# Performance work log

Measured on AMD Instinct MI355X. Metric: run time of the kernel, lower is better.

## Reference

```python
import jax, jax.numpy as jnp
import numpy as np

EPS = 1e-8


def setup_inputs() -> dict:
    key = jax.random.key(0)
    k1, k2, k3, k4 = jax.random.split(key, 4)
    B, D, K, L = 131072, 256, 1024, 526
    points = jax.random.normal(k1, (B, D), dtype=jnp.float32)
    labels = jax.random.uniform(k2, (B, L), dtype=jnp.float32)
    centroids = jax.random.normal(k3, (K, D), dtype=jnp.float32)
    running_labels = jax.random.uniform(k4, (K, L), dtype=jnp.float32)
    return {"points": points, "labels": labels, "centroids": centroids,
            "running_labels": running_labels}


def reference(points, labels, centroids, running_labels):
    # One kmeans step: assign -> compute_distance -> compute_distance_labels -> update
    K = centroids.shape[0]
    B = points.shape[0]
    # compute_similarity: squared euclidean distance (B, K), fused matmul form
    x2 = jnp.sum(points * points, axis=-1, keepdims=True)          # (B, 1)
    c2 = jnp.sum(centroids * centroids, axis=-1)                   # (K,)
    d = x2 - 2.0 * (points @ centroids.T) + c2                     # (B, K)
    assignment = jnp.argmin(d, axis=1)                             # (B,)

    # compute_distance: squared dist to assigned centroid + per-cluster dispersion
    sel = centroids[assignment]                                    # (B, D) gather
    dist = jnp.sum(jnp.square(sel - points), axis=-1)              # (B,)
    dispersion = jax.ops.segment_sum(dist, assignment, num_segments=K)

    # compute_distance_labels: cosine distance to assigned cluster label profile
    cl = running_labels[assignment]                                # (B, L) gather
    norm = jnp.sqrt(jnp.sum(jnp.square(labels), axis=-1))
    norm1 = jnp.sqrt(jnp.sum(jnp.square(cl), axis=-1))
    dist_labels = 1.0 - jnp.sum(cl * labels, axis=-1) / (norm * norm1 + EPS)
    dispersion_labels = jax.ops.segment_sum(dist_labels, assignment, num_segments=K)

    # update: scatter segment-sum running statistics
    new_sum = jax.ops.segment_sum(points, assignment, num_segments=K)   # (K, D)
    new_n = jax.ops.segment_sum(jnp.ones((B,), points.dtype), assignment, num_segments=K)
    new_labels = jax.ops.segment_sum(labels, assignment, num_segments=K)  # (K, L)

    return (assignment, dist, dispersion, dist_labels, dispersion_labels,
            new_sum, new_n, new_labels)
```

## Files before the change

kernel.cpp:

```cpp
#include <hip/hip_runtime.h>
#include <float.h>
#include <math.h>

constexpr int Bn = 131072;
constexpr int Dn = 256;
constexpr int Kn = 1024;
constexpr int Ln = 526;
constexpr float EPSF = 1e-8f;

constexpr int CHUNK = 128;
constexpr int MAXCHUNKS = Bn / CHUNK + Kn;

constexpr int BM  = 128;
constexpr int BN  = 128;
constexpr int KC  = 32;
constexpr int NT  = Kn / BN;
constexpr int KCH = Dn / KC;
constexpr int NCH = NT * KCH;
constexpr int LDH = 40;

typedef _Float16 f16x8 __attribute__((ext_vector_type(8)));
typedef _Float16 f16x4 __attribute__((ext_vector_type(4)));
typedef float    f32x4 __attribute__((ext_vector_type(4)));

union SMemU {
    _Float16 planes[2][4][BM][LDH];
    struct { float t[BM][2]; int k[BM][2]; } red;
};

__global__ __launch_bounds__(256) void prep_kernel(
    const float* __restrict__ centroids, const float* __restrict__ rlabels,
    float* __restrict__ c2, float* __restrict__ rln)
{
    const int k = blockIdx.x;
    const int t = threadIdx.x;
    float v = centroids[k * Dn + t];
    float s1 = v * v;
    float s2 = 0.f;
    for (int i = t; i < Ln; i += 256) {
        float u = rlabels[(size_t)k * Ln + i];
        s2 += u * u;
    }
    for (int off = 32; off > 0; off >>= 1) {
        s1 += __shfl_down(s1, off, 64);
        s2 += __shfl_down(s2, off, 64);
    }
    __shared__ float red[8];
    const int wv = t >> 6;
    if ((t & 63) == 0) { red[wv * 2] = s1; red[wv * 2 + 1] = s2; }
    __syncthreads();
    if (t == 0) {
        c2[k]  = red[0] + red[2] + red[4] + red[6];
        rln[k] = sqrtf(red[1] + red[3] + red[5] + red[7]);
    }
}

__global__ __launch_bounds__(256, 2) void assign_kernel(
    const float* __restrict__ points, const float* __restrict__ centroids,
    const float* __restrict__ c2,
    float* __restrict__ o_assign, int* __restrict__ ws_assign,
    float* __restrict__ ws_tmin)
{
    __shared__ __align__(16) SMemU sm;
    const int tid  = threadIdx.x;
    const int lane = tid & 63;
    const int wid  = tid >> 6;
    const int wrow = wid >> 1;
    const int wcol = wid & 1;
    const int ln15 = lane & 15;
    const int koff = (lane >> 4) * 8;
    const int bm0  = blockIdx.x * BM;

    f32x4 acc[4][4];
#pragma unroll
    for (int i = 0; i < 4; ++i)
#pragma unroll
        for (int j = 0; j < 4; ++j)
#pragma unroll
            for (int r = 0; r < 4; ++r) acc[i][j][r] = 0.f;

    float mint[16];
    int   mink[16];
#pragma unroll
    for (int s = 0; s < 16; ++s) { mint[s] = FLT_MAX; mink[s] = 0; }

    float4 pa[4], pb[4];
    auto prefetch = [&](int t) {
        const int nt = t >> 3, kc = t & 7;
        const int dof = kc * KC;
#pragma unroll
        for (int rep = 0; rep < 4; ++rep) {
            const int idx = rep * 256 + tid;
            const int row = idx >> 3;
            const int c4  = (idx & 7) * 4;
            pa[rep] = *(const float4*)(points    + (size_t)(bm0 + row) * Dn + dof + c4);
            pb[rep] = *(const float4*)(centroids + (size_t)(nt * BN + row) * Dn + dof + c4);
        }
    };
    auto writeLDS = [&](int buf) {
#pragma unroll
        for (int rep = 0; rep < 4; ++rep) {
            const int idx = rep * 256 + tid;
            const int row = idx >> 3;
            const int c4  = (idx & 7) * 4;
            float4 v = pa[rep];
            f16x4 h, l;
            h.x = (_Float16)v.x; l.x = (_Float16)(v.x - (float)h.x);
            h.y = (_Float16)v.y; l.y = (_Float16)(v.y - (float)h.y);
            h.z = (_Float16)v.z; l.z = (_Float16)(v.z - (float)h.z);
            h.w = (_Float16)v.w; l.w = (_Float16)(v.w - (float)h.w);
            *(f16x4*)&sm.planes[buf][0][row][c4] = h;
            *(f16x4*)&sm.planes[buf][1][row][c4] = l;
            v = pb[rep];
            h.x = (_Float16)v.x; l.x = (_Float16)(v.x - (float)h.x);
            h.y = (_Float16)v.y; l.y = (_Float16)(v.y - (float)h.y);
            h.z = (_Float16)v.z; l.z = (_Float16)(v.z - (float)h.z);
            h.w = (_Float16)v.w; l.w = (_Float16)(v.w - (float)h.w);
            *(f16x4*)&sm.planes[buf][2][row][c4] = h;
            *(f16x4*)&sm.planes[buf][3][row][c4] = l;
        }
    };

    prefetch(0);
    writeLDS(0);
    __syncthreads();

    for (int t = 0; t < NCH; ++t) {
        const int buf = t & 1;
        const bool more = (t + 1) < NCH;
        if (more) prefetch(t + 1);

        f16x8 ah[4], al[4], bh[4], bl[4];
#pragma unroll
        for (int mi = 0; mi < 4; ++mi) {
            const int ar = wrow * 64 + mi * 16 + ln15;
            ah[mi] = *(const f16x8*)&sm.planes[buf][0][ar][koff];
            al[mi] = *(const f16x8*)&sm.planes[buf][1][ar][koff];
        }
#pragma unroll
        for (int nj = 0; nj < 4; ++nj) {
            const int br = wcol * 64 + nj * 16 + ln15;
            bh[nj] = *(const f16x8*)&sm.planes[buf][2][br][koff];
            bl[nj] = *(const f16x8*)&sm.planes[buf][3][br][koff];
        }
#pragma unroll
        for (int mi = 0; mi < 4; ++mi)
#pragma unroll
            for (int nj = 0; nj < 4; ++nj) {
                acc[mi][nj] = __builtin_amdgcn_mfma_f32_16x16x32_f16(
                    al[mi], bh[nj], acc[mi][nj], 0, 0, 0);
                acc[mi][nj] = __builtin_amdgcn_mfma_f32_16x16x32_f16(
                    ah[mi], bl[nj], acc[mi][nj], 0, 0, 0);
                acc[mi][nj] = __builtin_amdgcn_mfma_f32_16x16x32_f16(
                    ah[mi], bh[nj], acc[mi][nj], 0, 0, 0);
            }

        if ((t & 7) == 7) {
            const int nt = t >> 3;
            const int nb = nt * BN + wcol * 64 + ln15;
#pragma unroll
            for (int nj = 0; nj < 4; ++nj) {
                const int n = nb + nj * 16;
                const float c2n = c2[n];
#pragma unroll
                for (int mi = 0; mi < 4; ++mi)
#pragma unroll
                    for (int r = 0; r < 4; ++r) {
                        const float tv = fmaf(-2.f, acc[mi][nj][r], c2n);
                        const int s = mi * 4 + r;
                        if (tv < mint[s] || (tv == mint[s] && n < mink[s])) {
                            mint[s] = tv; mink[s] = n;
                        }
                        acc[mi][nj][r] = 0.f;
                    }
            }
        }

        if (more) {
            writeLDS(buf ^ 1);
            __syncthreads();
        }
    }

#pragma unroll
    for (int s = 0; s < 16; ++s) {
        float tv = mint[s]; int kv = mink[s];
#pragma unroll
        for (int off = 1; off < 16; off <<= 1) {
            const float to = __shfl_xor(tv, off, 64);
            const int   ko = __shfl_xor(kv, off, 64);
            if (to < tv || (to == tv && ko < kv)) { tv = to; kv = ko; }
        }
        mint[s] = tv; mink[s] = kv;
    }
    __syncthreads();
    if (ln15 == 0) {
        const int g = lane >> 4;
#pragma unroll
        for (int s = 0; s < 16; ++s) {
            const int pr = wrow * 64 + (s >> 2) * 16 + g * 4 + (s & 3);
            sm.red.t[pr][wcol] = mint[s];
            sm.red.k[pr][wcol] = mink[s];
        }
    }
    __syncthreads();
    if (tid < BM) {
        float bt = sm.red.t[tid][0];
        int   bk = sm.red.k[tid][0];
        const float t1 = sm.red.t[tid][1];
        const int   k1 = sm.red.k[tid][1];
        if (t1 < bt || (t1 == bt && k1 < bk)) { bt = t1; bk = k1; }
        o_assign[bm0 + tid]  = (float)bk;
        ws_assign[bm0 + tid] = bk;
        ws_tmin[bm0 + tid]   = bt;
    }
}

__global__ __launch_bounds__(256) void count_kernel(
    const int* __restrict__ assigni, int* __restrict__ counts)
{
    const int p = blockIdx.x * 256 + threadIdx.x;
    atomicAdd(&counts[assigni[p]], 1);
}

__global__ __launch_bounds__(1024) void scan_kernel(
    const int* __restrict__ counts, int* __restrict__ offsets,
    int* __restrict__ cursor, float* __restrict__ o_nn,
    int* __restrict__ chunk_off)
{
    __shared__ int s[Kn];
    const int t = threadIdx.x;
    const int c = counts[t];
    o_nn[t] = (float)c;
    s[t] = c;
    __syncthreads();
    for (int off = 1; off < Kn; off <<= 1) {
        const int u = (t >= off) ? s[t - off] : 0;
        __syncthreads();
        s[t] += u;
        __syncthreads();
    }
    const int excl = s[t] - c;
    offsets[t] = excl;
    cursor[t]  = excl;

    const int cc = (c + CHUNK - 1) / CHUNK;
    __syncthreads();
    s[t] = cc;
    __syncthreads();
    for (int off = 1; off < Kn; off <<= 1) {
        const int u = (t >= off) ? s[t - off] : 0;
        __syncthreads();
        s[t] += u;
        __syncthreads();
    }
    chunk_off[t] = s[t] - cc;
    if (t == Kn - 1) chunk_off[Kn] = s[t];
}

__global__ __launch_bounds__(256) void scatter_kernel(
    const int* __restrict__ assigni, int* __restrict__ cursor,
    int* __restrict__ bucket)
{
    const int p = blockIdx.x * 256 + threadIdx.x;
    const int a = assigni[p];
    const int idx = atomicAdd(&cursor[a], 1);
    bucket[idx] = p;
}

__global__ __launch_bounds__(256) void fused_cluster_kernel(
    const float* __restrict__ points, const float* __restrict__ labels,
    const float* __restrict__ rlabels,
    const int* __restrict__ bucket, const int* __restrict__ offsets,
    const int* __restrict__ counts, const int* __restrict__ chunk_off,
    const float* __restrict__ tmin, const float* __restrict__ rln,
    float* __restrict__ o_dist, float* __restrict__ o_disp,
    float* __restrict__ o_dlab, float* __restrict__ o_displab,
    float* __restrict__ o_nsum, float* __restrict__ o_nlab)
{
    const int b = blockIdx.x;
    if (b >= chunk_off[Kn]) return;

    int lo = 0, hi = Kn;
    while (hi - lo > 1) {
        const int mid = (lo + hi) >> 1;
        if (chunk_off[mid] <= b) lo = mid; else hi = mid;
    }
    const int k   = lo;
    const int j   = b - chunk_off[k];
    const int nk  = counts[k];
    const int beg = offsets[k] + j * CHUNK;
    const int nm  = min(nk - j * CHUNK, CHUNK);
    const bool single = (nk <= CHUNK);

    const int tid  = threadIdx.x;
    const int lane = tid & 63;
    const int w    = tid >> 6;

    __shared__ int   sidx[CHUNK];
    __shared__ __align__(16) float srl[528];
    __shared__ float sacc[784];
    __shared__ float sdisp[4], sdlab[4];

    for (int i = tid; i < nm; i += 256) sidx[i] = bucket[beg + i];
    for (int i = tid; i < Ln; i += 256) srl[i] = rlabels[(size_t)k * Ln + i];
    for (int i = tid; i < 784; i += 256) sacc[i] = 0.f;
    __syncthreads();

    const float2 rl0 = *(const float2*)&srl[2 * lane];
    const float2 rl1 = *(const float2*)&srl[2 * (64 + lane)];
    const float2 rl2 = *(const float2*)&srl[2 * (128 + lane)];
    const float2 rl3 = *(const float2*)&srl[2 * (192 + lane)];
    float2 rlT = make_float2(0.f, 0.f);
    if (lane < 7) rlT = *(const float2*)&srl[2 * (256 + lane)];
    const float rlnk = rln[k];

    float4 accP  = make_float4(0.f, 0.f, 0.f, 0.f);
    float2 accL0 = make_float2(0.f, 0.f), accL1 = accL0,
           accL2 = accL0, accL3 = accL0, accLT = accL0;
    float dispacc = 0.f, displabacc = 0.f;

    float4 pv0; float2 a0, b0_, c0, d0, e0; int p0 = 0; float t0 = 0.f;
    auto loadM = [&](int i, float4& pv, float2& a, float2& bb, float2& cc,
                     float2& dd, float2& ee, int& pid, float& tm) {
        pid = sidx[i];
        pv = ((const float4*)(points + (size_t)pid * Dn))[lane];
        const float2* l2p = (const float2*)(labels + (size_t)pid * Ln);
        a  = l2p[lane];
        bb = l2p[64 + lane];
        cc = l2p[128 + lane];
        dd = l2p[192 + lane];
        ee = (lane < 7) ? l2p[256 + lane] : make_float2(0.f, 0.f);
        tm = (lane == 0) ? tmin[pid] : 0.f;
    };

    int i = w;
    if (i < nm) loadM(i, pv0, a0, b0_, c0, d0, e0, p0, t0);
    while (i < nm) {
        const int inext = i + 4;
        float4 pv1; float2 a1, b1_, c1, d1, e1; int p1 = 0; float t1 = 0.f;
        if (inext < nm) loadM(inext, pv1, a1, b1_, c1, d1, e1, p1, t1);

        accP.x += pv0.x; accP.y += pv0.y; accP.z += pv0.z; accP.w += pv0.w;
        accL0.x += a0.x;  accL0.y += a0.y;
        accL1.x += b0_.x; accL1.y += b0_.y;
        accL2.x += c0.x;  accL2.y += c0.y;
        accL3.x += d0.x;  accL3.y += d0.y;
        accLT.x += e0.x;  accLT.y += e0.y;

        float x2m = pv0.x * pv0.x + pv0.y * pv0.y + pv0.z * pv0.z + pv0.w * pv0.w;
        float l2m = a0.x * a0.x + a0.y * a0.y + b0_.x * b0_.x + b0_.y * b0_.y
                  + c0.x * c0.x + c0.y * c0.y + d0.x * d0.x + d0.y * d0.y
                  + e0.x * e0.x + e0.y * e0.y;
        float dtm = a0.x * rl0.x + a0.y * rl0.y + b0_.x * rl1.x + b0_.y * rl1.y
                  + c0.x * rl2.x + c0.y * rl2.y + d0.x * rl3.x + d0.y * rl3.y
                  + e0.x * rlT.x + e0.y * rlT.y;
#pragma unroll
        for (int off = 1; off < 64; off <<= 1) {
            x2m += __shfl_xor(x2m, off, 64);
            l2m += __shfl_xor(l2m, off, 64);
            dtm += __shfl_xor(dtm, off, 64);
        }
        if (lane == 0) {
            const float dist = x2m + t0;
            o_dist[p0] = dist;
            const float dl = 1.0f - dtm / (sqrtf(l2m) * rlnk + EPSF);
            o_dlab[p0] = dl;
            dispacc += dist;
            displabacc += dl;
        }

        pv0 = pv1; a0 = a1; b0_ = b1_; c0 = c1; d0 = d1; e0 = e1;
        p0 = p1; t0 = t1;
        i = inext;
    }

    if (lane == 0) { sdisp[w] = dispacc; sdlab[w] = displabacc; }

    for (int ww = 0; ww < 4; ++ww) {
        __syncthreads();
        if (w == ww) {
            float* sp = sacc;
            sp[4 * lane + 0] += accP.x;
            sp[4 * lane + 1] += accP.y;
            sp[4 * lane + 2] += accP.z;
            sp[4 * lane + 3] += accP.w;
            float* sl = sacc + 256;
            sl[2 * lane]           += accL0.x; sl[2 * lane + 1]       += accL0.y;
            sl[128 + 2 * lane]     += accL1.x; sl[128 + 2 * lane + 1] += accL1.y;
            sl[256 + 2 * lane]     += accL2.x; sl[256 + 2 * lane + 1] += accL2.y;
            sl[384 + 2 * lane]     += accL3.x; sl[384 + 2 * lane + 1] += accL3.y;
            if (lane < 7) {
                sl[512 + 2 * lane]     += accLT.x;
                sl[512 + 2 * lane + 1] += accLT.y;
            }
        }
    }
    __syncthreads();

    float* np = o_nsum + (size_t)k * Dn;
    float* nl = o_nlab + (size_t)k * Ln;
    const float vP  = sacc[tid];
    const float vL0 = sacc[256 + tid];
    const float vL1 = sacc[512 + tid];
    if (single) {
        np[tid]       = vP;
        nl[tid]       = vL0;
        nl[tid + 256] = vL1;
        if (tid < 14) nl[tid + 512] = sacc[768 + tid];
    } else {
        atomicAdd(&np[tid], vP);
        atomicAdd(&nl[tid], vL0);
        atomicAdd(&nl[tid + 256], vL1);
        if (tid < 14) atomicAdd(&nl[tid + 512], sacc[768 + tid]);
    }
    if (tid == 0) {
        const float dsum  = sdisp[0] + sdisp[1] + sdisp[2] + sdisp[3];
        const float dlsum = sdlab[0] + sdlab[1] + sdlab[2] + sdlab[3];
        if (single) { o_disp[k] = dsum; o_displab[k] = dlsum; }
        else { atomicAdd(&o_disp[k], dsum); atomicAdd(&o_displab[k], dlsum); }
    }
}

extern "C" void kernel_launch(void* const* d_in, const int* in_sizes, int n_in,
                              void* d_out, int out_size, void* d_ws, size_t ws_size,
                              hipStream_t stream)
{
    const float* points    = (const float*)d_in[0];
    const float* labels    = (const float*)d_in[1];
    const float* centroids = (const float*)d_in[2];
    const float* rlabels   = (const float*)d_in[3];

    float* out = (float*)d_out;
    float* o_assign  = out;
    float* o_dist    = out + Bn;
    float* o_disp    = out + 2 * Bn;
    float* o_dlab    = o_disp + Kn;
    float* o_displab = o_dlab + Bn;
    float* o_nsum    = o_displab + Kn;
    float* o_nn      = o_nsum + Kn * Dn;
    float* o_nlab    = o_nn + Kn;

    float* ws        = (float*)d_ws;
    float* c2        = ws;
    float* rln       = ws + Kn;
    float* tmin      = ws + 2 * Kn;
    int*   assigni   = (int*)(ws + 2 * Kn + Bn);
    int*   counts    = assigni + Bn;
    int*   offsets   = counts + Kn;
    int*   cursor    = offsets + Kn;
    int*   bucket    = cursor + Kn;
    int*   chunk_off = bucket + Bn;

    hipMemsetAsync(counts, 0, Kn * sizeof(int), stream);
    hipMemsetAsync(o_disp, 0, Kn * sizeof(float), stream);
    hipMemsetAsync(o_displab, 0, Kn * sizeof(float), stream);
    hipMemsetAsync(o_nsum, 0, (size_t)Kn * Dn * sizeof(float), stream);
    hipMemsetAsync(o_nlab, 0, (size_t)Kn * Ln * sizeof(float), stream);

    prep_kernel<<<Kn, 256, 0, stream>>>(centroids, rlabels, c2, rln);
    assign_kernel<<<Bn / BM, 256, 0, stream>>>(points, centroids, c2,
                                               o_assign, assigni, tmin);
    count_kernel<<<Bn / 256, 256, 0, stream>>>(assigni, counts);
    scan_kernel<<<1, Kn, 0, stream>>>(counts, offsets, cursor, o_nn, chunk_off);
    scatter_kernel<<<Bn / 256, 256, 0, stream>>>(assigni, cursor, bucket);
    fused_cluster_kernel<<<MAXCHUNKS, 256, 0, stream>>>(
        points, labels, rlabels, bucket, offsets, counts, chunk_off,
        tmin, rln, o_dist, o_disp, o_dlab, o_displab, o_nsum, o_nlab);
}
```

Before: 822.0 us.

## Pre-split centroids to fp16 planes and DMA them into swizzled LDS

```diff
diff --git a/kernel.cpp b/kernel.cpp
--- a/kernel.cpp
+++ b/kernel.cpp
@@ -17,24 +17,36 @@
 constexpr int NT  = Kn / BN;
 constexpr int KCH = Dn / KC;
 constexpr int NCH = NT * KCH;
-constexpr int LDH = 40;
 
 typedef _Float16 f16x8 __attribute__((ext_vector_type(8)));
 typedef _Float16 f16x4 __attribute__((ext_vector_type(4)));
 typedef float    f32x4 __attribute__((ext_vector_type(4)));
 
 union SMemU {
-    _Float16 planes[2][4][BM][LDH];
+    _Float16 tiles[2][2][BM][64];
     struct { float t[BM][2]; int k[BM][2]; } red;
 };
 
+__device__ __forceinline__ void dma16(const void* g, void* l) {
+    __builtin_amdgcn_global_load_lds(
+        (const __attribute__((address_space(1))) unsigned int*)g,
+        (__attribute__((address_space(3))) unsigned int*)l, 16, 0, 0);
+}
+
 __global__ __launch_bounds__(256) void prep_kernel(
     const float* __restrict__ centroids, const float* __restrict__ rlabels,
-    float* __restrict__ c2, float* __restrict__ rln)
+    float* __restrict__ c2, float* __restrict__ rln, _Float16* __restrict__ cpk)
 {
     const int k = blockIdx.x;
     const int t = threadIdx.x;
     float v = centroids[k * Dn + t];
+    {
+        const int c = t >> 5, j = t & 31;
+        const _Float16 h = (_Float16)v;
+        const _Float16 l = (_Float16)(v - (float)h);
+        cpk[((size_t)k * KCH + c) * 64 + j]      = h;
+        cpk[((size_t)k * KCH + c) * 64 + 32 + j] = l;
+    }
     float s1 = v * v;
     float s2 = 0.f;
     for (int i = t; i < Ln; i += 256) {
@@ -56,10 +68,10 @@
 }
 
 __global__ __launch_bounds__(256, 2) void assign_kernel(
-    const float* __restrict__ points, const float* __restrict__ centroids,
+    const float* __restrict__ points, const _Float16* __restrict__ cpk,
     const float* __restrict__ c2,
     float* __restrict__ o_assign, int* __restrict__ ws_assign,
-    float* __restrict__ ws_tmin)
+    float* __restrict__ ws_tmin, int* __restrict__ counts)
 {
     __shared__ __align__(16) SMemU sm;
     const int tid  = threadIdx.x;
@@ -68,8 +80,16 @@
     const int wrow = wid >> 1;
     const int wcol = wid & 1;
     const int ln15 = lane & 15;
-    const int koff = (lane >> 4) * 8;
+    const int g    = lane >> 4;
     const int bm0  = blockIdx.x * BM;
+
+    const int arow  = tid >> 1;
+    const int ahalf = tid & 1;
+    const int r7a   = arow & 7;
+    const int s0a   = ahalf * 2;
+
+    const int rowl = lane >> 3;
+    const int q8   = lane & 7;
 
     f32x4 acc[4][4];
 #pragma unroll
@@ -84,64 +104,71 @@
 #pragma unroll
     for (int s = 0; s < 16; ++s) { mint[s] = FLT_MAX; mink[s] = 0; }
 
-    float4 pa[4], pb[4];
-    auto prefetch = [&](int t) {
+    float4 pa[4];
+    auto loadA = [&](int t) {
+        const int kc = t & 7;
+        const float* ap = points + (size_t)(bm0 + arow) * Dn + kc * KC + ahalf * 16;
+        pa[0] = *(const float4*)(ap);
+        pa[1] = *(const float4*)(ap + 4);
+        pa[2] = *(const float4*)(ap + 8);
+        pa[3] = *(const float4*)(ap + 12);
+    };
+    auto dmaB = [&](int t, int buf) {
         const int nt = t >> 3, kc = t & 7;
-        const int dof = kc * KC;
-#pragma unroll
-        for (int rep = 0; rep < 4; ++rep) {
-            const int idx = rep * 256 + tid;
-            const int row = idx >> 3;
-            const int c4  = (idx & 7) * 4;
-            pa[rep] = *(const float4*)(points    + (size_t)(bm0 + row) * Dn + dof + c4);
-            pb[rep] = *(const float4*)(centroids + (size_t)(nt * BN + row) * Dn + dof + c4);
+#pragma unroll
+        for (int jj = 0; jj < 4; ++jj) {
+            const int p  = wid * 4 + jj;
+            const int br = p * 8 + rowl;
+            const int srcslot = q8 ^ (br & 7);
+            const _Float16* gp = cpk
+                + ((size_t)(nt * BN + br) * KCH + kc) * 64 + srcslot * 8;
+            dma16(gp, &sm.tiles[buf][1][p * 8][0]);
         }
     };
-    auto writeLDS = [&](int buf) {
-#pragma unroll
-        for (int rep = 0; rep < 4; ++rep) {
-            const int idx = rep * 256 + tid;
-            const int row = idx >> 3;
-            const int c4  = (idx & 7) * 4;
-            float4 v = pa[rep];
-            f16x4 h, l;
-            h.x = (_Float16)v.x; l.x = (_Float16)(v.x - (float)h.x);
-            h.y = (_Float16)v.y; l.y = (_Float16)(v.y - (float)h.y);
-            h.z = (_Float16)v.z; l.z = (_Float16)(v.z - (float)h.z);
-            h.w = (_Float16)v.w; l.w = (_Float16)(v.w - (float)h.w);
-            *(f16x4*)&sm.planes[buf][0][row][c4] = h;
-            *(f16x4*)&sm.planes[buf][1][row][c4] = l;
-            v = pb[rep];
-            h.x = (_Float16)v.x; l.x = (_Float16)(v.x - (float)h.x);
-            h.y = (_Float16)v.y; l.y = (_Float16)(v.y - (float)h.y);
-            h.z = (_Float16)v.z; l.z = (_Float16)(v.z - (float)h.z);
-            h.w = (_Float16)v.w; l.w = (_Float16)(v.w - (float)h.w);
-            *(f16x4*)&sm.planes[buf][2][row][c4] = h;
-            *(f16x4*)&sm.planes[buf][3][row][c4] = l;
-        }
+    auto writeA = [&](int buf) {
+        _Float16* Ar = &sm.tiles[buf][0][arow][0];
+        const float vs[16] = {pa[0].x, pa[0].y, pa[0].z, pa[0].w,
+                              pa[1].x, pa[1].y, pa[1].z, pa[1].w,
+                              pa[2].x, pa[2].y, pa[2].z, pa[2].w,
+                              pa[3].x, pa[3].y, pa[3].z, pa[3].w};
+        f16x8 h0, h1, l0, l1;
+#pragma unroll
+        for (int u = 0; u < 8; ++u) {
+            h0[u] = (_Float16)vs[u];     l0[u] = (_Float16)(vs[u]     - (float)h0[u]);
+            h1[u] = (_Float16)vs[8 + u]; l1[u] = (_Float16)(vs[8 + u] - (float)h1[u]);
+        }
+        *(f16x8*)&Ar[((s0a    ) ^ r7a) * 8] = h0;
+        *(f16x8*)&Ar[((s0a + 1) ^ r7a) * 8] = h1;
+        *(f16x8*)&Ar[((s0a + 4) ^ r7a) * 8] = l0;
+        *(f16x8*)&Ar[((s0a + 5) ^ r7a) * 8] = l1;
     };
 
-    prefetch(0);
-    writeLDS(0);
+    loadA(0);
+    dmaB(0, 0);
+    writeA(0);
     __syncthreads();
 
     for (int t = 0; t < NCH; ++t) {
         const int buf = t & 1;
         const bool more = (t + 1) < NCH;
-        if (more) prefetch(t + 1);
+        if (more) { loadA(t + 1); dmaB(t + 1, buf ^ 1); }
 
         f16x8 ah[4], al[4], bh[4], bl[4];
 #pragma unroll
         for (int mi = 0; mi < 4; ++mi) {
-            const int ar = wrow * 64 + mi * 16 + ln15;
-            ah[mi] = *(const f16x8*)&sm.planes[buf][0][ar][koff];
-            al[mi] = *(const f16x8*)&sm.planes[buf][1][ar][koff];
+            const int r  = wrow * 64 + mi * 16 + ln15;
+            const int r7 = r & 7;
+            const _Float16* Ar = &sm.tiles[buf][0][r][0];
+            ah[mi] = *(const f16x8*)&Ar[((g    ) ^ r7) * 8];
+            al[mi] = *(const f16x8*)&Ar[((g + 4) ^ r7) * 8];
         }
 #pragma unroll
         for (int nj = 0; nj < 4; ++nj) {
-            const int br = wcol * 64 + nj * 16 + ln15;
-            bh[nj] = *(const f16x8*)&sm.planes[buf][2][br][koff];
-            bl[nj] = *(const f16x8*)&sm.planes[buf][3][br][koff];
+            const int r  = wcol * 64 + nj * 16 + ln15;
+            const int r7 = r & 7;
+            const _Float16* Br = &sm.tiles[buf][1][r][0];
+            bh[nj] = *(const f16x8*)&Br[((g    ) ^ r7) * 8];
+            bl[nj] = *(const f16x8*)&Br[((g + 4) ^ r7) * 8];
         }
 #pragma unroll
         for (int mi = 0; mi < 4; ++mi)
@@ -177,7 +204,7 @@
         }
 
         if (more) {
-            writeLDS(buf ^ 1);
+            writeA(buf ^ 1);
             __syncthreads();
         }
     }
@@ -195,7 +222,6 @@
     }
     __syncthreads();
     if (ln15 == 0) {
-        const int g = lane >> 4;
 #pragma unroll
         for (int s = 0; s < 16; ++s) {
             const int pr = wrow * 64 + (s >> 2) * 16 + g * 4 + (s & 3);
@@ -213,14 +239,8 @@
         o_assign[bm0 + tid]  = (float)bk;
         ws_assign[bm0 + tid] = bk;
         ws_tmin[bm0 + tid]   = bt;
-    }
-}
-
-__global__ __launch_bounds__(256) void count_kernel(
-    const int* __restrict__ assigni, int* __restrict__ counts)
-{
-    const int p = blockIdx.x * 256 + threadIdx.x;
-    atomicAdd(&counts[assigni[p]], 1);
+        atomicAdd(&counts[bk], 1);
+    }
 }
 
 __global__ __launch_bounds__(1024) void scan_kernel(
@@ -320,7 +340,6 @@
            accL2 = accL0, accL3 = accL0, accLT = accL0;
     float dispacc = 0.f, displabacc = 0.f;
 
-    float4 pv0; float2 a0, b0_, c0, d0, e0; int p0 = 0; float t0 = 0.f;
     auto loadM = [&](int i, float4& pv, float2& a, float2& bb, float2& cc,
                      float2& dd, float2& ee, int& pid, float& tm) {
         pid = sidx[i];
@@ -334,12 +353,18 @@
         tm = (lane == 0) ? tmin[pid] : 0.f;
     };
 
+    float4 pv0 = make_float4(0,0,0,0), pv1 = pv0, pvX = pv0;
+    float2 z2 = make_float2(0.f, 0.f);
+    float2 a0 = z2, b0_ = z2, c0 = z2, d0 = z2, e0 = z2;
+    float2 a1 = z2, b1_ = z2, c1 = z2, d1 = z2, e1 = z2;
+    float2 aX = z2, bX_ = z2, cX = z2, dX = z2, eX = z2;
+    int p0 = 0, p1 = 0, pX = 0; float t0 = 0.f, t1 = 0.f, tX = 0.f;
+
     int i = w;
-    if (i < nm) loadM(i, pv0, a0, b0_, c0, d0, e0, p0, t0);
+    if (i < nm)     loadM(i,     pv0, a0, b0_, c0, d0, e0, p0, t0);
+    if (i + 4 < nm) loadM(i + 4, pv1, a1, b1_, c1, d1, e1, p1, t1);
     while (i < nm) {
-        const int inext = i + 4;
-        float4 pv1; float2 a1, b1_, c1, d1, e1; int p1 = 0; float t1 = 0.f;
-        if (inext < nm) loadM(inext, pv1, a1, b1_, c1, d1, e1, p1, t1);
+        if (i + 8 < nm) loadM(i + 8, pvX, aX, bX_, cX, dX, eX, pX, tX);
 
         accP.x += pv0.x; accP.y += pv0.y; accP.z += pv0.z; accP.w += pv0.w;
         accL0.x += a0.x;  accL0.y += a0.y;
@@ -370,30 +395,26 @@
             displabacc += dl;
         }
 
-        pv0 = pv1; a0 = a1; b0_ = b1_; c0 = c1; d0 = d1; e0 = e1;
-        p0 = p1; t0 = t1;
-        i = inext;
+        pv0 = pv1; a0 = a1; b0_ = b1_; c0 = c1; d0 = d1; e0 = e1; p0 = p1; t0 = t1;
+        pv1 = pvX; a1 = aX; b1_ = bX_; c1 = cX; d1 = dX; e1 = eX; p1 = pX; t1 = tX;
+        i += 4;
     }
 
     if (lane == 0) { sdisp[w] = dispacc; sdlab[w] = displabacc; }
 
-    for (int ww = 0; ww < 4; ++ww) {
-        __syncthreads();
-        if (w == ww) {
-            float* sp = sacc;
-            sp[4 * lane + 0] += accP.x;
-            sp[4 * lane + 1] += accP.y;
-            sp[4 * lane + 2] += accP.z;
-            sp[4 * lane + 3] += accP.w;
-            float* sl = sacc + 256;
-            sl[2 * lane]           += accL0.x; sl[2 * lane + 1]       += accL0.y;
-            sl[128 + 2 * lane]     += accL1.x; sl[128 + 2 * lane + 1] += accL1.y;
-            sl[256 + 2 * lane]     += accL2.x; sl[256 + 2 * lane + 1] += accL2.y;
-            sl[384 + 2 * lane]     += accL3.x; sl[384 + 2 * lane + 1] += accL3.y;
-            if (lane < 7) {
-                sl[512 + 2 * lane]     += accLT.x;
-                sl[512 + 2 * lane + 1] += accLT.y;
-            }
+    {
+        atomicAdd(&sacc[4 * lane + 0], accP.x);
+        atomicAdd(&sacc[4 * lane + 1], accP.y);
+        atomicAdd(&sacc[4 * lane + 2], accP.z);
+        atomicAdd(&sacc[4 * lane + 3], accP.w);
+        float* sl = sacc + 256;
+        atomicAdd(&sl[2 * lane],           accL0.x); atomicAdd(&sl[2 * lane + 1],       accL0.y);
+        atomicAdd(&sl[128 + 2 * lane],     accL1.x); atomicAdd(&sl[128 + 2 * lane + 1], accL1.y);
+        atomicAdd(&sl[256 + 2 * lane],     accL2.x); atomicAdd(&sl[256 + 2 * lane + 1], accL2.y);
+        atomicAdd(&sl[384 + 2 * lane],     accL3.x); atomicAdd(&sl[384 + 2 * lane + 1], accL3.y);
+        if (lane < 7) {
+            atomicAdd(&sl[512 + 2 * lane],     accLT.x);
+            atomicAdd(&sl[512 + 2 * lane + 1], accLT.y);
         }
     }
     __syncthreads();
@@ -451,6 +472,7 @@
     int*   cursor    = offsets + Kn;
     int*   bucket    = cursor + Kn;
     int*   chunk_off = bucket + Bn;
+    _Float16* cpk    = (_Float16*)(ws + 400000);
 
     hipMemsetAsync(counts, 0, Kn * sizeof(int), stream);
     hipMemsetAsync(o_disp, 0, Kn * sizeof(float), stream);
@@ -458,10 +480,9 @@
     hipMemsetAsync(o_nsum, 0, (size_t)Kn * Dn * sizeof(float), stream);
     hipMemsetAsync(o_nlab, 0, (size_t)Kn * Ln * sizeof(float), stream);
 
-    prep_kernel<<<Kn, 256, 0, stream>>>(centroids, rlabels, c2, rln);
-    assign_kernel<<<Bn / BM, 256, 0, stream>>>(points, centroids, c2,
-                                               o_assign, assigni, tmin);
-    count_kernel<<<Bn / 256, 256, 0, stream>>>(assigni, counts);
+    prep_kernel<<<Kn, 256, 0, stream>>>(centroids, rlabels, c2, rln, cpk);
+    assign_kernel<<<Bn / BM, 256, 0, stream>>>(points, cpk, c2,
+                                               o_assign, assigni, tmin, counts);
     scan_kernel<<<1, Kn, 0, stream>>>(counts, offsets, cursor, o_nn, chunk_off);
     scatter_kernel<<<Bn / 256, 256, 0, stream>>>(assigni, cursor, bucket);
     fused_cluster_kernel<<<MAXCHUNKS, 256, 0, stream>>>(
```

Measured after the change: 796.6 us. 3.1% less time.
